# Kernel tuning notes

Measured on AMD Instinct MI355X. Metric: run time of the kernel, lower is better.

Reference implementation:

```python
import jax, jax.numpy as jnp
import numpy as np

EMBED_DIM = 1024


def setup_inputs() -> dict:
    key = jax.random.key(0)
    ks = jax.random.split(key, 8)
    B, S, D = 4, 2048, EMBED_DIM
    scale = 1.0 / np.sqrt(D)
    x = jax.random.normal(ks[0], (B, S, D), dtype=jnp.float32)
    mask = jnp.zeros((S, S), dtype=jnp.float32)
    # nn.Linear default init ~ U(-1/sqrt(fan_in), 1/sqrt(fan_in)); exact dist irrelevant for correctness
    w_q = jax.random.uniform(ks[1], (D, D), jnp.float32, -scale, scale)
    b_q = jax.random.uniform(ks[2], (D,), jnp.float32, -scale, scale)
    w_k = jax.random.uniform(ks[3], (D, D), jnp.float32, -scale, scale)
    b_k = jax.random.uniform(ks[4], (D,), jnp.float32, -scale, scale)
    w_v = jax.random.uniform(ks[5], (D, D), jnp.float32, -scale, scale)
    b_v = jax.random.uniform(ks[6], (D,), jnp.float32, -scale, scale)
    return {"x": x, "mask": mask, "w_q": w_q, "b_q": b_q,
            "w_k": w_k, "b_k": b_k, "w_v": w_v, "b_v": b_v}


def reference(x, mask, w_q, b_q, w_k, b_k, w_v, b_v):
    D = x.shape[-1]
    # nn.Linear computes x @ W^T + b
    Q = jnp.einsum('bsd,ed->bse', x, w_q) + b_q
    K = jnp.einsum('bsd,ed->bse', x, w_k) + b_k
    V = jnp.einsum('bsd,ed->bse', x, w_v) + b_v
    scores = jnp.einsum('bqd,bkd->bqk', Q, K) / jnp.sqrt(jnp.asarray(D, x.dtype))
    scores = scores + mask  # additive mask, broadcast over batch
    attn = jax.nn.softmax(scores, axis=-1)
    return jnp.einsum('bqk,bkd->bqd', attn, V)
```

## Files before the change

kernel.cpp:

```cpp
#include <hip/hip_runtime.h>


typedef __attribute__((ext_vector_type(8))) short short8;
typedef __attribute__((ext_vector_type(4))) short short4v;
typedef __attribute__((ext_vector_type(4))) float float4v;

__device__ __forceinline__ short f2bf(float f) {
  unsigned u = __builtin_bit_cast(unsigned, f);
  u += 0x7fffu + ((u >> 16) & 1u);
  return (short)(u >> 16);
}
__device__ __forceinline__ float bf2f(short s) {
  unsigned u = ((unsigned)(unsigned short)s) << 16;
  return __builtin_bit_cast(float, u);
}

__device__ __forceinline__ void gl2lds16(const void* g, void* l) {
  __builtin_amdgcn_global_load_lds((const __attribute__((address_space(1))) void*)g,
                                   (__attribute__((address_space(3))) void*)l, 16, 0, 0);
}

__global__ __launch_bounds__(256) void prep_kernel(const float* __restrict__ x,
                                                   const float* __restrict__ wq,
                                                   const float* __restrict__ wk,
                                                   const float* __restrict__ wv,
                                                   const float* __restrict__ bq,
                                                   const float* __restrict__ bk,
                                                   short* __restrict__ x_bf,
                                                   short* __restrict__ w_bf,
                                                   float* __restrict__ bcat) {
  int b = blockIdx.x;
  if (b < 3072) {
    int seg = b >> 10;
    const float* w = seg == 0 ? wq : (seg == 1 ? wk : wv);
    int i = (b - (seg << 10)) * 256 + threadIdx.x;
    float4v v = ((const float4v*)w)[i];
    short4v o;
    o.x = f2bf(v.x); o.y = f2bf(v.y); o.z = f2bf(v.z); o.w = f2bf(v.w);
    ((short4v*)(w_bf + (long)seg * 1048576))[i] = o;
  } else if (b < 11264) {
    int i = (b - 3072) * 256 + threadIdx.x;
    float4v v = ((const float4v*)x)[i];
    short4v o;
    o.x = f2bf(v.x); o.y = f2bf(v.y); o.z = f2bf(v.z); o.w = f2bf(v.w);
    ((short4v*)x_bf)[i] = o;
  } else {
    int i = (b - 11264) * 256 + threadIdx.x;
    if (i < 2048) bcat[i] = i < 1024 ? bq[i] : bk[i - 1024];
  }
}

__device__ __forceinline__ void stage_half(const short* __restrict__ g, int ld,
                                           int grow0, int kt, short* lds, int t) {
  const int r = t >> 3;
  const int cch = (t & 7) ^ (r & 7);
  const long co = (long)kt + cch * 8;
  gl2lds16(g + (long)(grow0 + r) * ld + co, lds + t * 8);
  gl2lds16(g + (long)(grow0 + 64 + r) * ld + co, lds + 4096 + t * 8);
}

template <int EPI>
__device__ __forceinline__ void gemm_body(const short* __restrict__ A,
                                          const short* __restrict__ Bm,
                                          void* __restrict__ C,
                                          const float* __restrict__ aux,
                                          float* __restrict__ rsum, float scale,
                                          int N, int Kd, int Bld, int m0, int n0,
                                          short (*As)[64], short (*Bs)[64]) {
  const int t = threadIdx.x;
  const int lane = t & 63;
  const int wave = t >> 6;
  const int wm = (wave >> 2) * 128;
  const int wn = (wave & 3) * 64;
  const int col = lane & 15, quad = lane >> 4;
  const int sw = col & 7;
  const int NT = Kd >> 6;

  float4v acc[8][4] = {};

  stage_half(A, Kd, m0, 0, &As[0][0], t);
  stage_half(A, Kd, m0 + 128, 0, &As[128][0], t);
  stage_half(Bm, Bld, n0, 0, &Bs[0][0], t);
  stage_half(Bm, Bld, n0 + 128, 0, &Bs[128][0], t);
  if (NT > 1) {
    stage_half(A, Kd, m0, 64, &As[256][0], t);
    stage_half(A, Kd, m0 + 128, 64, &As[384][0], t);
    stage_half(Bm, Bld, n0, 64, &Bs[256][0], t);
    stage_half(Bm, Bld, n0 + 128, 64, &Bs[384][0], t);
    asm volatile("s_waitcnt vmcnt(8)" ::: "memory");
  } else {
    asm volatile("s_waitcnt vmcnt(0)" ::: "memory");
  }
  __builtin_amdgcn_s_barrier();

  int ar = 0;
  int aw = 512;
  int br = 0;

  for (int k = 0; k < NT; ++k) {
    short8 a[4][2], b0[2][2], b1[2][2];

#pragma unroll
    for (int i = 0; i < 4; ++i)
#pragma unroll
      for (int s = 0; s < 2; ++s)
        a[i][s] = *(const short8*)&As[ar + wm + i * 16 + col][(((s * 4 + quad) ^ sw)) * 8];
#pragma unroll
    for (int j = 0; j < 2; ++j)
#pragma unroll
      for (int s = 0; s < 2; ++s)
        b0[j][s] = *(const short8*)&Bs[br + wn + j * 16 + col][(((s * 4 + quad) ^ sw)) * 8];
    if (k + 2 < NT) stage_half(A, Kd, m0, (k + 2) * 64, &As[aw][0], t);
    __builtin_amdgcn_s_barrier();
    __builtin_amdgcn_s_setprio(1);
#pragma unroll
    for (int i = 0; i < 4; ++i)
#pragma unroll
      for (int j = 0; j < 2; ++j)
#pragma unroll
        for (int s = 0; s < 2; ++s)
          acc[i][j] = __builtin_amdgcn_mfma_f32_16x16x32_bf16(a[i][s], b0[j][s], acc[i][j], 0, 0, 0);
    __builtin_amdgcn_s_setprio(0);

#pragma unroll
    for (int j = 0; j < 2; ++j)
#pragma unroll
      for (int s = 0; s < 2; ++s)
        b1[j][s] = *(const short8*)&Bs[br + wn + (j + 2) * 16 + col][(((s * 4 + quad) ^ sw)) * 8];
    if (k + 2 < NT) stage_half(A, Kd, m0 + 128, (k + 2) * 64, &As[aw + 128][0], t);
    __builtin_amdgcn_s_barrier();
    __builtin_amdgcn_s_setprio(1);
#pragma unroll
    for (int i = 0; i < 4; ++i)
#pragma unroll
      for (int j = 0; j < 2; ++j)
#pragma unroll
        for (int s = 0; s < 2; ++s)
          acc[i][j + 2] = __builtin_amdgcn_mfma_f32_16x16x32_bf16(a[i][s], b1[j][s], acc[i][j + 2], 0, 0, 0);
    __builtin_amdgcn_s_setprio(0);

#pragma unroll
    for (int i = 0; i < 4; ++i)
#pragma unroll
      for (int s = 0; s < 2; ++s)
        a[i][s] = *(const short8*)&As[ar + wm + (i + 4) * 16 + col][(((s * 4 + quad) ^ sw)) * 8];
    if (k + 2 < NT) stage_half(Bm, Bld, n0, (k + 2) * 64, &Bs[br][0], t);
    __builtin_amdgcn_s_barrier();
    __builtin_amdgcn_s_setprio(1);
#pragma unroll
    for (int i = 0; i < 4; ++i)
#pragma unroll
      for (int j = 0; j < 2; ++j)
#pragma unroll
        for (int s = 0; s < 2; ++s)
          acc[i + 4][j + 2] = __builtin_amdgcn_mfma_f32_16x16x32_bf16(a[i][s], b1[j][s], acc[i + 4][j + 2], 0, 0, 0);
    __builtin_amdgcn_s_setprio(0);

    if (k + 2 < NT) stage_half(Bm, Bld, n0 + 128, (k + 2) * 64, &Bs[br + 128][0], t);
    if (k + 2 < NT) {
      asm volatile("s_waitcnt vmcnt(8)" ::: "memory");
    } else if (k + 1 < NT) {
      asm volatile("s_waitcnt vmcnt(0)" ::: "memory");
    }
    __builtin_amdgcn_s_barrier();
    __builtin_amdgcn_s_setprio(1);
#pragma unroll
    for (int i = 0; i < 4; ++i)
#pragma unroll
      for (int j = 0; j < 2; ++j)
#pragma unroll
        for (int s = 0; s < 2; ++s)
          acc[i + 4][j] = __builtin_amdgcn_mfma_f32_16x16x32_bf16(a[i][s], b0[j][s], acc[i + 4][j], 0, 0, 0);
    __builtin_amdgcn_s_setprio(0);

    ar = (ar == 512) ? 0 : ar + 256;
    aw = (aw == 512) ? 0 : aw + 256;
    br ^= 256;
  }

  float* invb = (float*)&Bs[0][0];
  if (EPI == 2) {
    __syncthreads();
    if (t < 256) {
      float s = 0.f;
#pragma unroll
      for (int p = 0; p < 32; ++p) s += aux[p * 8192 + m0 + t];
      invb[t] = __builtin_amdgcn_rcpf(s);
    }
    __syncthreads();
  }

  const float LOG2E = 1.44269504f;
  const float c1 = scale * LOG2E;
#pragma unroll
  for (int i = 0; i < 8; ++i) {
    float invv[4], addm[4], rsum4[4] = {0.f, 0.f, 0.f, 0.f};
    if (EPI == 2) {
#pragma unroll
      for (int r = 0; r < 4; ++r) invv[r] = invb[wm + i * 16 + quad * 4 + r];
    }
    if (EPI == 3) {
#pragma unroll
      for (int r = 0; r < 4; ++r) addm[r] = aux[m0 + wm + i * 16 + quad * 4 + r];
    }
#pragma unroll
    for (int j = 0; j < 4; ++j) {
      const int n = n0 + wn + j * 16 + col;
      float addn = 0.f;
      if (EPI == 0) addn = aux[n];
#pragma unroll
      for (int r = 0; r < 4; ++r) {
        const int m = m0 + wm + i * 16 + quad * 4 + r;
        float v = acc[i][j][r];
        if (EPI == 0) {
          ((short*)C)[(long)m * N + n] = f2bf(v + addn);
        } else if (EPI == 1) {
          float mv = aux[(long)m * N + n];
          float e = exp2f(fmaf(v, c1, mv * LOG2E));
          short q = f2bf(e);
          ((short*)C)[(long)m * N + n] = q;
          rsum4[r] += bf2f(q);
        } else if (EPI == 2) {
          ((float*)C)[(long)m * N + n] = v * invv[r];
        } else {
          ((short*)C)[(long)m * N + n] = f2bf(v + addm[r]);
        }
      }
    }
    if (EPI == 1) {
#pragma unroll
      for (int r = 0; r < 4; ++r) {
        float s = rsum4[r];
        s += __shfl_xor(s, 1);
        s += __shfl_xor(s, 2);
        s += __shfl_xor(s, 4);
        s += __shfl_xor(s, 8);
        if (col == 0)
          rsum[(wave & 3) * 8192 + m0 + wm + i * 16 + quad * 4 + r] = s;
      }
    }
  }
}

__global__ __launch_bounds__(512, 2) void qkv_kernel(const short* __restrict__ x_bf,
                                                     const short* __restrict__ w_bf,
                                                     short* __restrict__ QK,
                                                     short* __restrict__ Vt,
                                                     const float* __restrict__ bcat,
                                                     const float* __restrict__ bv) {
  __shared__ alignas(16) short As[768][64];
  __shared__ alignas(16) short Bs[512][64];
  const int b = blockIdx.x;
  const int g = (b & 7) * 48 + (b >> 3);
  if (g < 256) {
    const int bz = g >> 7, r = g & 127;
    const int m0 = (r >> 2) * 256, n0 = (r & 3) * 256;
    gemm_body<0>(x_bf, w_bf + (long)bz * 1048576, QK + (long)bz * 8388608,
                 bcat + bz * 1024, nullptr, 1.f, 1024, 1024, 1024, m0, n0, As, Bs);
  } else {
    const int v = g - 256;
    const int m0 = (v >> 5) * 256, n0 = (v & 31) * 256;
    gemm_body<3>(w_bf + 2097152, x_bf, Vt, bv, nullptr, 1.f,
                 8192, 1024, 1024, m0, n0, As, Bs);
  }
}

__global__ __launch_bounds__(512, 2) void scores_kernel(const short* __restrict__ Q,
                                                        const short* __restrict__ Kb,
                                                        short* __restrict__ P,
                                                        const float* __restrict__ mask,
                                                        float* __restrict__ rspart) {
  __shared__ alignas(16) short As[768][64];
  __shared__ alignas(16) short Bs[512][64];
  const int b = blockIdx.x;
  const int g = (b & 7) * 32 + (b >> 3);
  const int bz = g >> 6, t2 = g & 63;
  const int m0 = (t2 >> 3) * 256, n0 = (t2 & 7) * 256;
  gemm_body<1>(Q + (long)bz * 2097152, Kb + (long)bz * 2097152,
               P + (long)bz * 4194304, mask,
               rspart + (long)(n0 >> 8) * 4 * 8192 + bz * 2048, 0.03125f,
               2048, 1024, 1024, m0, n0, As, Bs);
}

__global__ __launch_bounds__(512, 2) void pv_kernel(const short* __restrict__ P,
                                                    const short* __restrict__ Vt,
                                                    float* __restrict__ out,
                                                    const float* __restrict__ rspart) {
  __shared__ alignas(16) short As[768][64];
  __shared__ alignas(16) short Bs[512][64];
  const int b = blockIdx.x;
  const int g = (b & 7) * 16 + (b >> 3);
  const int bz = g >> 5, t2 = g & 31;
  const int m0 = (t2 >> 2) * 256, n0 = (t2 & 3) * 256;
  gemm_body<2>(P + (long)bz * 4194304, Vt + (long)bz * 2048,
               out + (long)bz * 2097152, rspart + bz * 2048, nullptr, 1.f,
               1024, 2048, 8192, m0, n0, As, Bs);
}

extern "C" void kernel_launch(void* const* d_in, const int* in_sizes, int n_in,
                              void* d_out, int out_size, void* d_ws, size_t ws_size,
                              hipStream_t stream) {
  const float* x    = (const float*)d_in[0];
  const float* mask = (const float*)d_in[1];
  const float* wq   = (const float*)d_in[2];
  const float* bq   = (const float*)d_in[3];
  const float* wk   = (const float*)d_in[4];
  const float* bk   = (const float*)d_in[5];
  const float* wv   = (const float*)d_in[6];
  const float* bv   = (const float*)d_in[7];
  float* out = (float*)d_out;

  char* ws = (char*)d_ws;
  const size_t MB = 1024 * 1024;
  short* x_bf   = (short*)(ws);
  float* rspart = (float*)(ws);
  short* w_bf   = (short*)(ws + 16 * MB);
  short* QK     = (short*)(ws + 22 * MB);
  short* Vt     = (short*)(ws + 54 * MB);
  short* P      = (short*)(ws + 70 * MB);
  float* bcat   = (float*)(ws + 70 * MB);

  prep_kernel<<<11272, 256, 0, stream>>>(x, wq, wk, wv, bq, bk, x_bf, w_bf, bcat);

  qkv_kernel<<<384, 512, 0, stream>>>(x_bf, w_bf, QK, Vt, bcat, bv);

  short* Q  = QK;
  short* Kb = QK + 8388608;

  scores_kernel<<<256, 512, 0, stream>>>(Q, Kb, P, mask, rspart);

  pv_kernel<<<128, 512, 0, stream>>>(P, Vt, out, rspart);
}
```

Measured before the change: 265.6 us.

## Add half-height M tile variant to fill all CUs in V-proj and PV GEMMs

Templates the GEMM body on the M tile height, adding a 128x256 tile path with its own two-stage pipeline schedule and wait counts. The V projection and the P·V GEMM now use the smaller tile, doubling their block counts (V blocks 128->256, pv 128->256) so more CUs are occupied. The cost is less operand reuse per block and more redundant B-tile loads.

```diff
diff --git a/kernel.cpp b/kernel.cpp
--- a/kernel.cpp
+++ b/kernel.cpp
@@ -59,7 +59,7 @@
   gl2lds16(g + (long)(grow0 + 64 + r) * ld + co, lds + 4096 + t * 8);
 }
 
-template <int EPI>
+template <int EPI, int MH>
 __device__ __forceinline__ void gemm_body(const short* __restrict__ A,
                                           const short* __restrict__ Bm,
                                           void* __restrict__ C,
@@ -70,118 +70,169 @@
   const int t = threadIdx.x;
   const int lane = t & 63;
   const int wave = t >> 6;
-  const int wm = (wave >> 2) * 128;
+  const int wm = (wave >> 2) * 64 * MH;
   const int wn = (wave & 3) * 64;
   const int col = lane & 15, quad = lane >> 4;
   const int sw = col & 7;
   const int NT = Kd >> 6;
-
-  float4v acc[8][4] = {};
+  constexpr int AS = 128 * MH;
+
+  float4v acc[4 * MH][4] = {};
 
   stage_half(A, Kd, m0, 0, &As[0][0], t);
-  stage_half(A, Kd, m0 + 128, 0, &As[128][0], t);
+  if constexpr (MH == 2) stage_half(A, Kd, m0 + 128, 0, &As[128][0], t);
   stage_half(Bm, Bld, n0, 0, &Bs[0][0], t);
   stage_half(Bm, Bld, n0 + 128, 0, &Bs[128][0], t);
   if (NT > 1) {
-    stage_half(A, Kd, m0, 64, &As[256][0], t);
-    stage_half(A, Kd, m0 + 128, 64, &As[384][0], t);
+    stage_half(A, Kd, m0, 64, &As[AS][0], t);
+    if constexpr (MH == 2) stage_half(A, Kd, m0 + 128, 64, &As[AS + 128][0], t);
     stage_half(Bm, Bld, n0, 64, &Bs[256][0], t);
     stage_half(Bm, Bld, n0 + 128, 64, &Bs[384][0], t);
-    asm volatile("s_waitcnt vmcnt(8)" ::: "memory");
+    if constexpr (MH == 2)
+      asm volatile("s_waitcnt vmcnt(8)" ::: "memory");
+    else
+      asm volatile("s_waitcnt vmcnt(6)" ::: "memory");
   } else {
     asm volatile("s_waitcnt vmcnt(0)" ::: "memory");
   }
   __builtin_amdgcn_s_barrier();
 
   int ar = 0;
-  int aw = 512;
+  int aw = 2 * AS;
   int br = 0;
 
   for (int k = 0; k < NT; ++k) {
     short8 a[4][2], b0[2][2], b1[2][2];
 
-#pragma unroll
-    for (int i = 0; i < 4; ++i)
-#pragma unroll
-      for (int s = 0; s < 2; ++s)
-        a[i][s] = *(const short8*)&As[ar + wm + i * 16 + col][(((s * 4 + quad) ^ sw)) * 8];
-#pragma unroll
-    for (int j = 0; j < 2; ++j)
-#pragma unroll
-      for (int s = 0; s < 2; ++s)
-        b0[j][s] = *(const short8*)&Bs[br + wn + j * 16 + col][(((s * 4 + quad) ^ sw)) * 8];
-    if (k + 2 < NT) stage_half(A, Kd, m0, (k + 2) * 64, &As[aw][0], t);
-    __builtin_amdgcn_s_barrier();
-    __builtin_amdgcn_s_setprio(1);
-#pragma unroll
-    for (int i = 0; i < 4; ++i)
+    if constexpr (MH == 2) {
+#pragma unroll
+      for (int i = 0; i < 4; ++i)
+#pragma unroll
+        for (int s = 0; s < 2; ++s)
+          a[i][s] = *(const short8*)&As[ar + wm + i * 16 + col][(((s * 4 + quad) ^ sw)) * 8];
 #pragma unroll
       for (int j = 0; j < 2; ++j)
 #pragma unroll
         for (int s = 0; s < 2; ++s)
-          acc[i][j] = __builtin_amdgcn_mfma_f32_16x16x32_bf16(a[i][s], b0[j][s], acc[i][j], 0, 0, 0);
-    __builtin_amdgcn_s_setprio(0);
-
-#pragma unroll
-    for (int j = 0; j < 2; ++j)
-#pragma unroll
-      for (int s = 0; s < 2; ++s)
-        b1[j][s] = *(const short8*)&Bs[br + wn + (j + 2) * 16 + col][(((s * 4 + quad) ^ sw)) * 8];
-    if (k + 2 < NT) stage_half(A, Kd, m0 + 128, (k + 2) * 64, &As[aw + 128][0], t);
-    __builtin_amdgcn_s_barrier();
-    __builtin_amdgcn_s_setprio(1);
-#pragma unroll
-    for (int i = 0; i < 4; ++i)
+          b0[j][s] = *(const short8*)&Bs[br + wn + j * 16 + col][(((s * 4 + quad) ^ sw)) * 8];
+      if (k + 2 < NT) stage_half(A, Kd, m0, (k + 2) * 64, &As[aw][0], t);
+      __builtin_amdgcn_s_barrier();
+      __builtin_amdgcn_s_setprio(1);
+#pragma unroll
+      for (int i = 0; i < 4; ++i)
+#pragma unroll
+        for (int j = 0; j < 2; ++j)
+#pragma unroll
+          for (int s = 0; s < 2; ++s)
+            acc[i][j] = __builtin_amdgcn_mfma_f32_16x16x32_bf16(a[i][s], b0[j][s], acc[i][j], 0, 0, 0);
+      __builtin_amdgcn_s_setprio(0);
+
 #pragma unroll
       for (int j = 0; j < 2; ++j)
 #pragma unroll
         for (int s = 0; s < 2; ++s)
-          acc[i][j + 2] = __builtin_amdgcn_mfma_f32_16x16x32_bf16(a[i][s], b1[j][s], acc[i][j + 2], 0, 0, 0);
-    __builtin_amdgcn_s_setprio(0);
-
-#pragma unroll
-    for (int i = 0; i < 4; ++i)
-#pragma unroll
-      for (int s = 0; s < 2; ++s)
-        a[i][s] = *(const short8*)&As[ar + wm + (i + 4) * 16 + col][(((s * 4 + quad) ^ sw)) * 8];
-    if (k + 2 < NT) stage_half(Bm, Bld, n0, (k + 2) * 64, &Bs[br][0], t);
-    __builtin_amdgcn_s_barrier();
-    __builtin_amdgcn_s_setprio(1);
-#pragma unroll
-    for (int i = 0; i < 4; ++i)
+          b1[j][s] = *(const short8*)&Bs[br + wn + (j + 2) * 16 + col][(((s * 4 + quad) ^ sw)) * 8];
+      if (k + 2 < NT) stage_half(A, Kd, m0 + 128, (k + 2) * 64, &As[aw + 128][0], t);
+      __builtin_amdgcn_s_barrier();
+      __builtin_amdgcn_s_setprio(1);
+#pragma unroll
+      for (int i = 0; i < 4; ++i)
+#pragma unroll
+        for (int j = 0; j < 2; ++j)
+#pragma unroll
+          for (int s = 0; s < 2; ++s)
+            acc[i][j + 2] = __builtin_amdgcn_mfma_f32_16x16x32_bf16(a[i][s], b1[j][s], acc[i][j + 2], 0, 0, 0);
+      __builtin_amdgcn_s_setprio(0);
+
+#pragma unroll
+      for (int i = 0; i < 4; ++i)
+#pragma unroll
+        for (int s = 0; s < 2; ++s)
+          a[i][s] = *(const short8*)&As[ar + wm + (i + 4) * 16 + col][(((s * 4 + quad) ^ sw)) * 8];
+      if (k + 2 < NT) stage_half(Bm, Bld, n0, (k + 2) * 64, &Bs[br][0], t);
+      __builtin_amdgcn_s_barrier();
+      __builtin_amdgcn_s_setprio(1);
+#pragma unroll
+      for (int i = 0; i < 4; ++i)
+#pragma unroll
+        for (int j = 0; j < 2; ++j)
+#pragma unroll
+          for (int s = 0; s < 2; ++s)
+            acc[i + 4][j + 2] = __builtin_amdgcn_mfma_f32_16x16x32_bf16(a[i][s], b1[j][s], acc[i + 4][j + 2], 0, 0, 0);
+      __builtin_amdgcn_s_setprio(0);
+
+      if (k + 2 < NT) stage_half(Bm, Bld, n0 + 128, (k + 2) * 64, &Bs[br + 128][0], t);
+      if (k + 2 < NT) {
+        asm volatile("s_waitcnt vmcnt(8)" ::: "memory");
+      } else if (k + 1 < NT) {
+        asm volatile("s_waitcnt vmcnt(0)" ::: "memory");
+      }
+      __builtin_amdgcn_s_barrier();
+      __builtin_amdgcn_s_setprio(1);
+#pragma unroll
+      for (int i = 0; i < 4; ++i)
+#pragma unroll
+        for (int j = 0; j < 2; ++j)
+#pragma unroll
+          for (int s = 0; s < 2; ++s)
+            acc[i + 4][j] = __builtin_amdgcn_mfma_f32_16x16x32_bf16(a[i][s], b0[j][s], acc[i + 4][j], 0, 0, 0);
+      __builtin_amdgcn_s_setprio(0);
+    } else {
+#pragma unroll
+      for (int i = 0; i < 4; ++i)
+#pragma unroll
+        for (int s = 0; s < 2; ++s)
+          a[i][s] = *(const short8*)&As[ar + wm + i * 16 + col][(((s * 4 + quad) ^ sw)) * 8];
 #pragma unroll
       for (int j = 0; j < 2; ++j)
 #pragma unroll
         for (int s = 0; s < 2; ++s)
-          acc[i + 4][j + 2] = __builtin_amdgcn_mfma_f32_16x16x32_bf16(a[i][s], b1[j][s], acc[i + 4][j + 2], 0, 0, 0);
-    __builtin_amdgcn_s_setprio(0);
-
-    if (k + 2 < NT) stage_half(Bm, Bld, n0 + 128, (k + 2) * 64, &Bs[br + 128][0], t);
-    if (k + 2 < NT) {
-      asm volatile("s_waitcnt vmcnt(8)" ::: "memory");
-    } else if (k + 1 < NT) {
-      asm volatile("s_waitcnt vmcnt(0)" ::: "memory");
-    }
-    __builtin_amdgcn_s_barrier();
-    __builtin_amdgcn_s_setprio(1);
-#pragma unroll
-    for (int i = 0; i < 4; ++i)
+          b0[j][s] = *(const short8*)&Bs[br + wn + j * 16 + col][(((s * 4 + quad) ^ sw)) * 8];
+      if (k + 2 < NT) stage_half(A, Kd, m0, (k + 2) * 64, &As[aw][0], t);
+      __builtin_amdgcn_s_barrier();
+      __builtin_amdgcn_s_setprio(1);
+#pragma unroll
+      for (int i = 0; i < 4; ++i)
+#pragma unroll
+        for (int j = 0; j < 2; ++j)
+#pragma unroll
+          for (int s = 0; s < 2; ++s)
+            acc[i][j] = __builtin_amdgcn_mfma_f32_16x16x32_bf16(a[i][s], b0[j][s], acc[i][j], 0, 0, 0);
+      __builtin_amdgcn_s_setprio(0);
+
 #pragma unroll
       for (int j = 0; j < 2; ++j)
 #pragma unroll
         for (int s = 0; s < 2; ++s)
-          acc[i + 4][j] = __builtin_amdgcn_mfma_f32_16x16x32_bf16(a[i][s], b0[j][s], acc[i + 4][j], 0, 0, 0);
-    __builtin_amdgcn_s_setprio(0);
-
-    ar = (ar == 512) ? 0 : ar + 256;
-    aw = (aw == 512) ? 0 : aw + 256;
+          b1[j][s] = *(const short8*)&Bs[br + wn + (j + 2) * 16 + col][(((s * 4 + quad) ^ sw)) * 8];
+      if (k + 2 < NT) {
+        stage_half(Bm, Bld, n0, (k + 2) * 64, &Bs[br][0], t);
+        stage_half(Bm, Bld, n0 + 128, (k + 2) * 64, &Bs[br + 128][0], t);
+        asm volatile("s_waitcnt vmcnt(6)" ::: "memory");
+      } else if (k + 1 < NT) {
+        asm volatile("s_waitcnt vmcnt(0)" ::: "memory");
+      }
+      __builtin_amdgcn_s_barrier();
+      __builtin_amdgcn_s_setprio(1);
+#pragma unroll
+      for (int i = 0; i < 4; ++i)
+#pragma unroll
+        for (int j = 0; j < 2; ++j)
+#pragma unroll
+          for (int s = 0; s < 2; ++s)
+            acc[i][j + 2] = __builtin_amdgcn_mfma_f32_16x16x32_bf16(a[i][s], b1[j][s], acc[i][j + 2], 0, 0, 0);
+      __builtin_amdgcn_s_setprio(0);
+    }
+
+    ar = (ar == 2 * AS) ? 0 : ar + AS;
+    aw = (aw == 2 * AS) ? 0 : aw + AS;
     br ^= 256;
   }
 
   float* invb = (float*)&Bs[0][0];
   if (EPI == 2) {
     __syncthreads();
-    if (t < 256) {
+    if (t < 128 * MH) {
       float s = 0.f;
 #pragma unroll
       for (int p = 0; p < 32; ++p) s += aux[p * 8192 + m0 + t];
@@ -193,7 +244,7 @@
   const float LOG2E = 1.44269504f;
   const float c1 = scale * LOG2E;
 #pragma unroll
-  for (int i = 0; i < 8; ++i) {
+  for (int i = 0; i < 4 * MH; ++i) {
     float invv[4], addm[4], rsum4[4] = {0.f, 0.f, 0.f, 0.f};
     if (EPI == 2) {
 #pragma unroll
@@ -251,17 +302,17 @@
   __shared__ alignas(16) short As[768][64];
   __shared__ alignas(16) short Bs[512][64];
   const int b = blockIdx.x;
-  const int g = (b & 7) * 48 + (b >> 3);
+  const int g = (b & 7) * 64 + (b >> 3);
   if (g < 256) {
     const int bz = g >> 7, r = g & 127;
     const int m0 = (r >> 2) * 256, n0 = (r & 3) * 256;
-    gemm_body<0>(x_bf, w_bf + (long)bz * 1048576, QK + (long)bz * 8388608,
-                 bcat + bz * 1024, nullptr, 1.f, 1024, 1024, 1024, m0, n0, As, Bs);
+    gemm_body<0, 2>(x_bf, w_bf + (long)bz * 1048576, QK + (long)bz * 8388608,
+                    bcat + bz * 1024, nullptr, 1.f, 1024, 1024, 1024, m0, n0, As, Bs);
   } else {
     const int v = g - 256;
-    const int m0 = (v >> 5) * 256, n0 = (v & 31) * 256;
-    gemm_body<3>(w_bf + 2097152, x_bf, Vt, bv, nullptr, 1.f,
-                 8192, 1024, 1024, m0, n0, As, Bs);
+    const int m0 = (v >> 5) * 128, n0 = (v & 31) * 256;
+    gemm_body<3, 1>(w_bf + 2097152, x_bf, Vt, bv, nullptr, 1.f,
+                    8192, 1024, 1024, m0, n0, As, Bs);
   }
 }
 
@@ -276,25 +327,25 @@
   const int g = (b & 7) * 32 + (b >> 3);
   const int bz = g >> 6, t2 = g & 63;
   const int m0 = (t2 >> 3) * 256, n0 = (t2 & 7) * 256;
-  gemm_body<1>(Q + (long)bz * 2097152, Kb + (long)bz * 2097152,
-               P + (long)bz * 4194304, mask,
-               rspart + (long)(n0 >> 8) * 4 * 8192 + bz * 2048, 0.03125f,
-               2048, 1024, 1024, m0, n0, As, Bs);
+  gemm_body<1, 2>(Q + (long)bz * 2097152, Kb + (long)bz * 2097152,
+                  P + (long)bz * 4194304, mask,
+                  rspart + (long)(n0 >> 8) * 4 * 8192 + bz * 2048, 0.03125f,
+                  2048, 1024, 1024, m0, n0, As, Bs);
 }
 
 __global__ __launch_bounds__(512, 2) void pv_kernel(const short* __restrict__ P,
                                                     const short* __restrict__ Vt,
                                                     float* __restrict__ out,
                                                     const float* __restrict__ rspart) {
-  __shared__ alignas(16) short As[768][64];
+  __shared__ alignas(16) short As[384][64];
   __shared__ alignas(16) short Bs[512][64];
   const int b = blockIdx.x;
-  const int g = (b & 7) * 16 + (b >> 3);
-  const int bz = g >> 5, t2 = g & 31;
-  const int m0 = (t2 >> 2) * 256, n0 = (t2 & 3) * 256;
-  gemm_body<2>(P + (long)bz * 4194304, Vt + (long)bz * 2048,
-               out + (long)bz * 2097152, rspart + bz * 2048, nullptr, 1.f,
-               1024, 2048, 8192, m0, n0, As, Bs);
+  const int g = (b & 7) * 32 + (b >> 3);
+  const int bz = g >> 6, t2 = g & 63;
+  const int m0 = (t2 >> 2) * 128, n0 = (t2 & 3) * 256;
+  gemm_body<2, 1>(P + (long)bz * 4194304, Vt + (long)bz * 2048,
+                  out + (long)bz * 2097152, rspart + bz * 2048, nullptr, 1.f,
+                  1024, 2048, 8192, m0, n0, As, Bs);
 }
 
 extern "C" void kernel_launch(void* const* d_in, const int* in_sizes, int n_in,
@@ -322,12 +373,12 @@
 
   prep_kernel<<<11272, 256, 0, stream>>>(x, wq, wk, wv, bq, bk, x_bf, w_bf, bcat);
 
-  qkv_kernel<<<384, 512, 0, stream>>>(x_bf, w_bf, QK, Vt, bcat, bv);
+  qkv_kernel<<<512, 512, 0, stream>>>(x_bf, w_bf, QK, Vt, bcat, bv);
 
   short* Q  = QK;
   short* Kb = QK + 8388608;
 
   scores_kernel<<<256, 512, 0, stream>>>(Q, Kb, P, mask, rspart);
 
-  pv_kernel<<<128, 512, 0, stream>>>(P, Vt, out, rspart);
-}
+  pv_kernel<<<256, 512, 0, stream>>>(P, Vt, out, rspart);
+}
```

Result: faster. 255.3 us (-3.8%).
